# Performance work log

Hardware: AMD Instinct MI355X
Metric: run time of the kernel (lower is better)

The kernel has to match this reference:

```python
import jax, jax.numpy as jnp
import numpy as np

N = 50000      # nodes
E = 800000     # edges
D_IN = 128     # embedding_in
EP = 200000    # prediction edge pairs
CONV_DIMS = [D_IN, 128, 64, 32]
LIN_DIMS = [32, 16, 8, 1]


def setup_inputs() -> dict:
    key = jax.random.key(0)
    ks = jax.random.split(key, 20)
    inp = {
        "x": jax.random.normal(ks[0], (N, D_IN), dtype=jnp.float32),
        "edge_index": jax.random.randint(ks[1], (2, E), 0, N, dtype=jnp.int64 if jax.config.jax_enable_x64 else jnp.int32),
        "pred_edges": jax.random.randint(ks[2], (EP, 2), 0, N, dtype=jnp.int64 if jax.config.jax_enable_x64 else jnp.int32),
    }
    k = 3
    for i in range(3):  # GCNConv weights [in,out] + bias (torch GCNConv has bias)
        din, dout = CONV_DIMS[i], CONV_DIMS[i + 1]
        inp[f"cw{i}"] = jax.random.normal(ks[k], (din, dout), dtype=jnp.float32) / np.sqrt(din); k += 1
        inp[f"cb{i}"] = jax.random.normal(ks[k], (dout,), dtype=jnp.float32) * 0.01; k += 1
    for i in range(3):  # Linear weights stored [in,out]
        din, dout = LIN_DIMS[i], LIN_DIMS[i + 1]
        inp[f"lw{i}"] = jax.random.normal(ks[k], (din, dout), dtype=jnp.float32) / np.sqrt(din); k += 1
        inp[f"lb{i}"] = jax.random.normal(ks[k], (dout,), dtype=jnp.float32) * 0.01; k += 1
    return inp


def gcn_conv(x, W, b, src, dst, n):
    """PyG GCNConv: D^-1/2 (A + I) D^-1/2 X W + b, deg over dst incl. self-loop."""
    h = x @ W  # [n, dout]
    deg = jax.ops.segment_sum(jnp.ones_like(dst, dtype=h.dtype), dst, num_segments=n) + 1.0
    dis = jax.lax.rsqrt(deg)  # deg >= 1 (self loop)
    msg = h[src] * (dis[src] * dis[dst])[:, None]      # gather + per-edge normalize
    out = jax.ops.segment_sum(msg, dst, num_segments=n)  # scatter-add into targets
    out = out + h * (dis * dis)[:, None]                # self-loop contribution
    return out + b


def reference(x, edge_index, pred_edges, cw0, cb0, cw1, cb1, cw2, cb2,
              lw0, lb0, lw1, lb1, lw2, lb2):
    src, dst = edge_index[0], edge_index[1]
    n = x.shape[0]
    for W, b in ((cw0, cb0), (cw1, cb1), (cw2, cb2)):
        x = jax.nn.relu(gcn_conv(x, W, b, src, dst, n))
    x = jax.nn.relu(x @ lw0 + lb0)
    x = jax.nn.relu(x @ lw1 + lb1)
    x = jax.nn.sigmoid(x @ lw2 + lb2)  # [n, 1]
    s = x[:, 0]
    # x[pred_edges] -> [EP,2,1]; mul of pair, transpose+flatten -> [EP]
    return s[pred_edges[:, 0]] * s[pred_edges[:, 1]]
```

## Files before the change

### kernel.cpp

```cpp
#include <hip/hip_runtime.h>
#include <math.h>

constexpr int NN  = 50000;
constexpr int NP  = 50048;
constexpr int NE  = 800000;
constexpr int NEP = 200000;

constexpr int NBKT  = 256;
constexpr int CAP   = 4096;
constexpr int CAPC  = 4096;
constexpr int CHUNK = 4096;

constexpr int BKB = (NE + CHUNK - 1) / CHUNK;
constexpr int W0B = 128 * 128 / 256;
constexpr int W1B = 128 * 64 / 256;
constexpr int W2B = 64 * 32 / 256;
constexpr int FRONT_BLOCKS = BKB + W0B + W1B + W2B;

constexpr int NODE_BLKS32 = (NN + 31) / 32;
constexpr int NODE_BLKS16 = (NN + 15) / 16;

typedef _Float16 half8_t __attribute__((ext_vector_type(8)));
typedef float    float4_t __attribute__((ext_vector_type(4)));

static inline int cdiv(long long a, int b) { return (int)((a + b - 1) / b); }

__global__ __launch_bounds__(256) void k_front(const int* __restrict__ src,
        const int* __restrict__ dst, int* __restrict__ binCnt,
        unsigned int* __restrict__ ebuf,
        const float* __restrict__ cw0, _Float16* __restrict__ WT0,
        const float* __restrict__ cw1, _Float16* __restrict__ WT1,
        const float* __restrict__ cw2, _Float16* __restrict__ WT2) {
    const int tid = threadIdx.x;
    const int bid = blockIdx.x;

    if (bid < BKB) {
        __shared__ int hist[NBKT];
        __shared__ int base[NBKT];
        __shared__ int cur[NBKT];
        constexpr int J = CHUNK / 256;
        const int e0 = bid * CHUNK;
        hist[tid] = 0;
        __syncthreads();
        int  s[J], bn[J], dl[J];
        bool ok[J];
#pragma unroll
        for (int j = 0; j < J; ++j) {
            int i = e0 + j * 256 + tid;
            ok[j] = i < NE;
            if (ok[j]) {
                int d = dst[i];
                s[j]  = src[i];
                bn[j] = d >> 8;
                dl[j] = d & 255;
                atomicAdd(&hist[bn[j]], 1);
            }
        }
        __syncthreads();
        base[tid] = hist[tid] ? atomicAdd(&binCnt[tid], hist[tid]) : 0;
        cur[tid] = 0;
        __syncthreads();
#pragma unroll
        for (int j = 0; j < J; ++j) {
            if (ok[j]) {
                int slot = base[bn[j]] + atomicAdd(&cur[bn[j]], 1);
                ebuf[bn[j] * CAP + slot] = (unsigned int)s[j] | ((unsigned int)dl[j] << 16);
            }
        }
        return;
    }
    if (bid < BKB + W0B) {
        int idx = (bid - BKB) * 256 + tid;
        int k = idx >> 7, n = idx & 127;
        WT0[(size_t)n * 128 + k] = (_Float16)cw0[idx];
        return;
    }
    if (bid < BKB + W0B + W1B) {
        int idx = (bid - BKB - W0B) * 256 + tid;
        int k = idx >> 6, n = idx & 63;
        WT1[(size_t)n * 128 + k] = (_Float16)cw1[idx];
        return;
    }
    {
        int idx = (bid - BKB - W0B - W1B) * 256 + tid;
        int k = idx >> 5, n = idx & 31;
        WT2[(size_t)n * 64 + k] = (_Float16)cw2[idx];
    }
}

__global__ __launch_bounds__(256) void k_csrbuild(const unsigned int* __restrict__ ebuf,
        const int* __restrict__ binCnt, int* __restrict__ off, float* __restrict__ dis,
        unsigned short* __restrict__ csr) {
    __shared__ int hist[256];
    __shared__ int sh[256];
    __shared__ int cur[256];
    const int tid = threadIdx.x;
    const int bin = blockIdx.x;
    const int cnt = binCnt[bin];
    const unsigned int* eb = ebuf + (size_t)bin * CAP;

    hist[tid] = 0;
    __syncthreads();
    for (int i = tid; i < cnt; i += 256)
        atomicAdd(&hist[eb[i] >> 16], 1);
    __syncthreads();

    int v  = hist[tid];
    int pv = (v + 3) & ~3;
    sh[tid] = pv;
    __syncthreads();
    for (int d = 1; d < 256; d <<= 1) {
        int t = (tid >= d) ? sh[tid - d] : 0;
        __syncthreads();
        sh[tid] += t;
        __syncthreads();
    }
    int start = bin * CAPC + (sh[tid] - pv);

    int node = bin * 256 + tid;
    if (node < NN) {
        off[node] = start | (pv << 20);
        dis[node] = rsqrtf((float)v + 1.0f);
    }
    cur[tid] = start;
    __syncthreads();

    for (int i = tid; i < cnt; i += 256) {
        unsigned int e = eb[i];
        int p = atomicAdd(&cur[e >> 16], 1);
        csr[p] = (unsigned short)(e & 0xFFFFu);
    }
    for (int k2 = v; k2 < pv; ++k2) csr[start + k2] = (unsigned short)NN;
}

__global__ __launch_bounds__(256) void k_gemm0(const float* __restrict__ X,
        const _Float16* __restrict__ WT, const float* __restrict__ dis,
        _Float16* __restrict__ g, int n) {
    constexpr int K = 128, DOUT = 128;
    constexpr int NC = 64, NT = 4, KT = 4, MT = 2;

    const int tid  = threadIdx.x;
    const int L    = tid & 63;
    const int w    = tid >> 6;
    const int wc   = w & 1;
    const int wr   = w >> 1;
    const int r0   = blockIdx.x * 64 + wr * 32;
    const int c0   = wc * NC;
    const int quad = L >> 4;
    const int lm   = L & 15;

    float4_t acc[MT][NT];
#pragma unroll
    for (int mt = 0; mt < MT; ++mt)
#pragma unroll
        for (int nt = 0; nt < NT; ++nt) acc[mt][nt] = (float4_t){0.f, 0.f, 0.f, 0.f};

#pragma unroll
    for (int kt = 0; kt < KT; ++kt) {
        half8_t a[MT], b[NT];
#pragma unroll
        for (int mt = 0; mt < MT; ++mt) {
            const float* xr = X + (size_t)(r0 + mt * 16 + lm) * K + kt * 32 + quad * 8;
            float4 u = *(const float4*)xr;
            float4 v = *(const float4*)(xr + 4);
            a[mt] = (half8_t){(_Float16)u.x, (_Float16)u.y, (_Float16)u.z, (_Float16)u.w,
                              (_Float16)v.x, (_Float16)v.y, (_Float16)v.z, (_Float16)v.w};
        }
#pragma unroll
        for (int nt = 0; nt < NT; ++nt)
            b[nt] = *(const half8_t*)(WT + (size_t)(c0 + nt * 16 + lm) * K + kt * 32 + quad * 8);
#pragma unroll
        for (int mt = 0; mt < MT; ++mt)
#pragma unroll
            for (int nt = 0; nt < NT; ++nt)
                acc[mt][nt] = __builtin_amdgcn_mfma_f32_16x16x32_f16(a[mt], b[nt], acc[mt][nt], 0, 0, 0);
    }

#pragma unroll
    for (int mt = 0; mt < MT; ++mt) {
        int rb = r0 + mt * 16 + quad * 4;
        float dv[4];
        *(float4*)dv = *(const float4*)(dis + rb);
#pragma unroll
        for (int nt = 0; nt < NT; ++nt) {
            int c = c0 + nt * 16 + lm;
#pragma unroll
            for (int reg = 0; reg < 4; ++reg) {
                int r = rb + reg;
                if (r < n)       g[(size_t)r * DOUT + c] = (_Float16)(acc[mt][nt][reg] * dv[reg]);
                else if (r == n) g[(size_t)r * DOUT + c] = (_Float16)0.f;
            }
        }
    }
}

__global__ __launch_bounds__(256) void k_agg_gemm16(const half8_t* __restrict__ gin,
        const float* __restrict__ dis, const float* __restrict__ bias,
        const int* __restrict__ off, const unsigned short* __restrict__ csr,
        const _Float16* __restrict__ WT, _Float16* __restrict__ gout, int n) {
    constexpr int DIN = 128, DOUT = 64;
    constexpr int R8 = DIN / 8;
    constexpr int XS = DIN + 8;
    __shared__ _Float16 sX[16 * XS];

    const int tid  = threadIdx.x;
    const int l16  = tid & 15;
    const int ln   = tid >> 4;
    const int r0   = blockIdx.x * 16;
    const int node = r0 + ln;

    if (blockIdx.x == 0 && tid < DOUT / 8)
        ((half8_t*)(gout + (size_t)n * DOUT))[tid] =
            (half8_t){(_Float16)0.f, (_Float16)0.f, (_Float16)0.f, (_Float16)0.f,
                      (_Float16)0.f, (_Float16)0.f, (_Float16)0.f, (_Float16)0.f};

    float dd = dis[node];
    half8_t hv = gin[(size_t)node * R8 + l16];
    float a[8];
#pragma unroll
    for (int j = 0; j < 8; ++j) a[j] = (float)hv[j];

    int pk = off[node];
    int e0 = pk & 0xFFFFF;
    int e1 = e0 + (pk >> 20);
    int e = e0;
    for (; e + 7 < e1; e += 8) {
        ushort4 c4 = *(const ushort4*)(csr + e);
        ushort4 c8 = *(const ushort4*)(csr + e + 4);
        half8_t v0 = gin[(size_t)c4.x * R8 + l16];
        half8_t v1 = gin[(size_t)c4.y * R8 + l16];
        half8_t v2 = gin[(size_t)c4.z * R8 + l16];
        half8_t v3 = gin[(size_t)c4.w * R8 + l16];
        half8_t v4 = gin[(size_t)c8.x * R8 + l16];
        half8_t v5 = gin[(size_t)c8.y * R8 + l16];
        half8_t v6 = gin[(size_t)c8.z * R8 + l16];
        half8_t v7 = gin[(size_t)c8.w * R8 + l16];
#pragma unroll
        for (int j = 0; j < 8; ++j)
            a[j] += ((float)v0[j] + (float)v1[j]) + ((float)v2[j] + (float)v3[j])
                  + ((float)v4[j] + (float)v5[j]) + ((float)v6[j] + (float)v7[j]);
    }
    if (e < e1) {
        ushort4 c4 = *(const ushort4*)(csr + e);
        half8_t v0 = gin[(size_t)c4.x * R8 + l16];
        half8_t v1 = gin[(size_t)c4.y * R8 + l16];
        half8_t v2 = gin[(size_t)c4.z * R8 + l16];
        half8_t v3 = gin[(size_t)c4.w * R8 + l16];
#pragma unroll
        for (int j = 0; j < 8; ++j)
            a[j] += ((float)v0[j] + (float)v1[j]) + ((float)v2[j] + (float)v3[j]);
    }
    {
        half8_t o;
#pragma unroll
        for (int j = 0; j < 8; ++j)
            o[j] = (_Float16)fmaxf(fmaf(a[j], dd, bias[l16 * 8 + j]), 0.f);
        *(half8_t*)(sX + ln * XS + l16 * 8) = o;
    }
    __syncthreads();

    const int L    = tid & 63;
    const int w    = tid >> 6;
    const int quad = L >> 4;
    const int lm   = L & 15;
    const int c0   = w * 16;

    float4_t acc = (float4_t){0.f, 0.f, 0.f, 0.f};
#pragma unroll
    for (int kt = 0; kt < DIN / 32; ++kt) {
        half8_t b  = *(const half8_t*)(WT + (size_t)(c0 + lm) * DIN + kt * 32 + quad * 8);
        half8_t aF = *(const half8_t*)(sX + lm * XS + kt * 32 + quad * 8);
        acc = __builtin_amdgcn_mfma_f32_16x16x32_f16(aF, b, acc, 0, 0, 0);
    }
    int rb = r0 + quad * 4;
    float dv[4];
    *(float4*)dv = *(const float4*)(dis + rb);
#pragma unroll
    for (int reg = 0; reg < 4; ++reg)
        gout[(size_t)(rb + reg) * DOUT + c0 + lm] = (_Float16)(acc[reg] * dv[reg]);
}

__global__ __launch_bounds__(256) void k_agg_gemm8(const half8_t* __restrict__ gin,
        const float* __restrict__ dis, const float* __restrict__ bias,
        const int* __restrict__ off, const unsigned short* __restrict__ csr,
        const _Float16* __restrict__ WT, _Float16* __restrict__ gout, int n) {
    constexpr int DIN = 64, DOUT = 32;
    constexpr int R8 = DIN / 8;
    constexpr int XS = DIN + 8;
    __shared__ _Float16 sX[32 * XS];

    const int tid  = threadIdx.x;
    const int l8   = tid & 7;
    const int ln   = tid >> 3;
    const int r0   = blockIdx.x * 32;
    const int node = r0 + ln;

    if (node < n) {
        float dd = dis[node];
        half8_t hv = gin[(size_t)node * R8 + l8];
        float a[8];
#pragma unroll
        for (int j = 0; j < 8; ++j) a[j] = (float)hv[j];
        int pk = off[node];
        int e0 = pk & 0xFFFFF;
        int e1 = e0 + (pk >> 20);
        int e = e0;
        for (; e + 7 < e1; e += 8) {
            ushort4 c4 = *(const ushort4*)(csr + e);
            ushort4 c8 = *(const ushort4*)(csr + e + 4);
            half8_t v0 = gin[(size_t)c4.x * R8 + l8];
            half8_t v1 = gin[(size_t)c4.y * R8 + l8];
            half8_t v2 = gin[(size_t)c4.z * R8 + l8];
            half8_t v3 = gin[(size_t)c4.w * R8 + l8];
            half8_t v4 = gin[(size_t)c8.x * R8 + l8];
            half8_t v5 = gin[(size_t)c8.y * R8 + l8];
            half8_t v6 = gin[(size_t)c8.z * R8 + l8];
            half8_t v7 = gin[(size_t)c8.w * R8 + l8];
#pragma unroll
            for (int j = 0; j < 8; ++j)
                a[j] += ((float)v0[j] + (float)v1[j]) + ((float)v2[j] + (float)v3[j])
                      + ((float)v4[j] + (float)v5[j]) + ((float)v6[j] + (float)v7[j]);
        }
        if (e < e1) {
            ushort4 c4 = *(const ushort4*)(csr + e);
            half8_t v0 = gin[(size_t)c4.x * R8 + l8];
            half8_t v1 = gin[(size_t)c4.y * R8 + l8];
            half8_t v2 = gin[(size_t)c4.z * R8 + l8];
            half8_t v3 = gin[(size_t)c4.w * R8 + l8];
#pragma unroll
            for (int j = 0; j < 8; ++j)
                a[j] += ((float)v0[j] + (float)v1[j]) + ((float)v2[j] + (float)v3[j]);
        }
        half8_t o;
#pragma unroll
        for (int j = 0; j < 8; ++j)
            o[j] = (_Float16)fmaxf(fmaf(a[j], dd, bias[l8 * 8 + j]), 0.f);
        *(half8_t*)(sX + ln * XS + l8 * 8) = o;
    } else {
        *(half8_t*)(sX + ln * XS + l8 * 8) =
            (half8_t){(_Float16)0.f, (_Float16)0.f, (_Float16)0.f, (_Float16)0.f,
                      (_Float16)0.f, (_Float16)0.f, (_Float16)0.f, (_Float16)0.f};
    }
    __syncthreads();

    const int L    = tid & 63;
    const int w    = tid >> 6;
    const int quad = L >> 4;
    const int lm   = L & 15;
    const int c0   = (w & 1) * 16;
    const int m0   = (w >> 1) * 16;

    float4_t acc = (float4_t){0.f, 0.f, 0.f, 0.f};
#pragma unroll
    for (int kt = 0; kt < DIN / 32; ++kt) {
        half8_t b  = *(const half8_t*)(WT + (size_t)(c0 + lm) * DIN + kt * 32 + quad * 8);
        half8_t aF = *(const half8_t*)(sX + (m0 + lm) * XS + kt * 32 + quad * 8);
        acc = __builtin_amdgcn_mfma_f32_16x16x32_f16(aF, b, acc, 0, 0, 0);
    }
    int rb = r0 + m0 + quad * 4;
    float dv[4];
    *(float4*)dv = *(const float4*)(dis + rb);
#pragma unroll
    for (int reg = 0; reg < 4; ++reg) {
        int r = rb + reg;
        if (r < n)       gout[(size_t)r * DOUT + c0 + lm] = (_Float16)(acc[reg] * dv[reg]);
        else if (r == n) gout[(size_t)r * DOUT + c0 + lm] = (_Float16)0.f;
    }
}

__global__ __launch_bounds__(256) void k_agg_mlp(const half8_t* __restrict__ g,
        const float* __restrict__ dis, const float* __restrict__ b,
        const int* __restrict__ off, const unsigned short* __restrict__ csr,
        const float* __restrict__ lw0, const float* __restrict__ lb0,
        const float* __restrict__ lw1, const float* __restrict__ lb1,
        const float* __restrict__ lw2, const float* __restrict__ lb2,
        float* __restrict__ sv, int n) {
    __shared__ float sh[32 * 33];
    const int tid  = threadIdx.x;
    const int l8   = tid & 7;
    const int lane = l8 & 3;
    const int grp  = l8 >> 2;
    const int ln   = tid >> 3;
    const int node = blockIdx.x * 32 + ln;

    if (node < n) {
        float dd = dis[node];
        half8_t hv = g[(size_t)node * 4 + lane];
        float a[8];
#pragma unroll
        for (int j = 0; j < 8; ++j) a[j] = (grp == 0) ? (float)hv[j] : 0.f;
        int pk = off[node];
        int e0 = pk & 0xFFFFF;
        int e1 = e0 + (pk >> 20);
        for (int e = e0 + grp * 4; e < e1; e += 8) {
            ushort4 c4 = *(const ushort4*)(csr + e);
            half8_t v0 = g[(size_t)c4.x * 4 + lane];
            half8_t v1 = g[(size_t)c4.y * 4 + lane];
            half8_t v2 = g[(size_t)c4.z * 4 + lane];
            half8_t v3 = g[(size_t)c4.w * 4 + lane];
#pragma unroll
            for (int j = 0; j < 8; ++j)
                a[j] += (float)v0[j] + (float)v1[j] + (float)v2[j] + (float)v3[j];
        }
#pragma unroll
        for (int j = 0; j < 8; ++j) a[j] += __shfl_xor(a[j], 4);
        if (grp == 0) {
            float* row = sh + ln * 33 + lane * 8;
#pragma unroll
            for (int j = 0; j < 8; ++j)
                row[j] = fmaxf(fmaf(a[j], dd, b[lane * 8 + j]), 0.f);
        }
    }
    __syncthreads();

    if (tid < 32) {
        int node2 = blockIdx.x * 32 + tid;
        if (node2 < n) {
            const float* v = sh + tid * 33;
            float a[16];
#pragma unroll
            for (int j = 0; j < 16; ++j) {
                float acc = lb0[j];
#pragma unroll
                for (int k = 0; k < 32; ++k) acc = fmaf(v[k], lw0[k * 16 + j], acc);
                a[j] = fmaxf(acc, 0.f);
            }
            float b8[8];
#pragma unroll
            for (int j = 0; j < 8; ++j) {
                float acc = lb1[j];
#pragma unroll
                for (int k = 0; k < 16; ++k) acc = fmaf(a[k], lw1[k * 8 + j], acc);
                b8[j] = fmaxf(acc, 0.f);
            }
            float z = lb2[0];
#pragma unroll
            for (int k = 0; k < 8; ++k) z = fmaf(b8[k], lw2[k], z);
            sv[node2] = 1.0f / (1.0f + expf(-z));
        }
    }
}

__global__ void k_pred(const float* __restrict__ s, const int* __restrict__ pe,
                       float* __restrict__ out, int ep2) {
    int i = blockIdx.x * blockDim.x + threadIdx.x;
    if (i >= ep2) return;
    int4 p = ((const int4*)pe)[i];
    float2 o;
    o.x = s[p.x] * s[p.y];
    o.y = s[p.z] * s[p.w];
    ((float2*)out)[i] = o;
}

extern "C" void kernel_launch(void* const* d_in, const int* in_sizes, int n_in,
                              void* d_out, int out_size, void* d_ws, size_t ws_size,
                              hipStream_t stream) {
    const float* x   = (const float*)d_in[0];
    const int*   ei  = (const int*)d_in[1];
    const int*   pe  = (const int*)d_in[2];
    const float* cw0 = (const float*)d_in[3];
    const float* cb0 = (const float*)d_in[4];
    const float* cw1 = (const float*)d_in[5];
    const float* cb1 = (const float*)d_in[6];
    const float* cw2 = (const float*)d_in[7];
    const float* cb2 = (const float*)d_in[8];
    const float* lw0 = (const float*)d_in[9];
    const float* lb0 = (const float*)d_in[10];
    const float* lw1 = (const float*)d_in[11];
    const float* lb1 = (const float*)d_in[12];
    const float* lw2 = (const float*)d_in[13];
    const float* lb2 = (const float*)d_in[14];

    const int* src = ei;
    const int* dst = ei + NE;

    char* w = (char*)d_ws;
    float*          dis  = (float*)w;           w += sizeof(float) * NN;
    _Float16*       M0   = (_Float16*)w;        w += sizeof(_Float16) * (size_t)(NN + 1) * 128;
    _Float16*       M1   = (_Float16*)w;        w += sizeof(_Float16) * (size_t)(NN + 1) * 64;
    _Float16*       M2   = (_Float16*)w;        w += sizeof(_Float16) * (size_t)(NN + 1) * 32;
    float*          sv   = (float*)w;           w += sizeof(float) * NN;
    _Float16*       WT0  = (_Float16*)w;        w += sizeof(_Float16) * 128 * 128;
    _Float16*       WT1  = (_Float16*)w;        w += sizeof(_Float16) * 64 * 128;
    _Float16*       WT2  = (_Float16*)w;        w += sizeof(_Float16) * 32 * 64;
    int*            off  = (int*)w;             w += sizeof(int) * NN;
    unsigned short* csr  = (unsigned short*)w;  w += sizeof(unsigned short) * (size_t)NBKT * CAPC;
    int*            binCnt = (int*)w;           w += sizeof(int) * NBKT;
    unsigned int*   ebuf = (unsigned int*)w;    w += sizeof(unsigned int) * (size_t)NBKT * CAP;

    const int T = 256;

    hipMemsetAsync(binCnt, 0, sizeof(int) * NBKT, stream);
    k_front<<<FRONT_BLOCKS, 256, 0, stream>>>(src, dst, binCnt, ebuf,
                                              cw0, WT0, cw1, WT1, cw2, WT2);

    k_csrbuild<<<NBKT, 256, 0, stream>>>(ebuf, binCnt, off, dis, csr);

    k_gemm0<<<NP / 64, 256, 0, stream>>>(x, WT0, dis, M0, NN);

    k_agg_gemm16<<<NODE_BLKS16, 256, 0, stream>>>((const half8_t*)M0, dis, cb0,
                                                  off, csr, WT1, M1, NN);

    k_agg_gemm8<<<NODE_BLKS32, 256, 0, stream>>>((const half8_t*)M1, dis, cb1,
                                                 off, csr, WT2, M2, NN);

    k_agg_mlp<<<NODE_BLKS32, 256, 0, stream>>>((const half8_t*)M2, dis, cb2, off, csr,
                                               lw0, lb0, lw1, lb1, lw2, lb2, sv, NN);

    k_pred<<<cdiv(NEP / 2, T), T, 0, stream>>>(sv, pe, (float*)d_out, NEP / 2);
}
```

Measured before the change: 213.2 us.

## Renumber nodes by in-degree so aggregation warps get balanced neighbor counts

Adds a degree histogram in the CSR build plus two new kernels that rank nodes by in-degree (counting sort) and remap CSR neighbor ids into the permuted numbering. gemm0 writes rows in permuted order, the aggregation kernels index the permuted offsets and scaling arrays, and the final MLP scatters back to original node ids. The aim is to group nodes of similar degree in the same wavefront, cutting divergence and load imbalance in the gather loops. The cost is two extra launches, a full pass over the CSR, and scattered writes in gemm0 and the MLP output.

```diff
diff --git a/kernel.cpp b/kernel.cpp
--- a/kernel.cpp
+++ b/kernel.cpp
@@ -19,6 +19,7 @@
 
 constexpr int NODE_BLKS32 = (NN + 31) / 32;
 constexpr int NODE_BLKS16 = (NN + 15) / 16;
+constexpr int NDEG = 128;
 
 typedef _Float16 half8_t __attribute__((ext_vector_type(8)));
 typedef float    float4_t __attribute__((ext_vector_type(4)));
@@ -90,16 +91,19 @@
 
 __global__ __launch_bounds__(256) void k_csrbuild(const unsigned int* __restrict__ ebuf,
         const int* __restrict__ binCnt, int* __restrict__ off, float* __restrict__ dis,
-        unsigned short* __restrict__ csr) {
+        unsigned short* __restrict__ csr, unsigned char* __restrict__ deg8,
+        int* __restrict__ degHist) {
     __shared__ int hist[256];
     __shared__ int sh[256];
     __shared__ int cur[256];
+    __shared__ int dh[NDEG];
     const int tid = threadIdx.x;
     const int bin = blockIdx.x;
     const int cnt = binCnt[bin];
     const unsigned int* eb = ebuf + (size_t)bin * CAP;
 
     hist[tid] = 0;
+    if (tid < NDEG) dh[tid] = 0;
     __syncthreads();
     for (int i = tid; i < cnt; i += 256)
         atomicAdd(&hist[eb[i] >> 16], 1);
@@ -121,6 +125,9 @@
     if (node < NN) {
         off[node] = start | (pv << 20);
         dis[node] = rsqrtf((float)v + 1.0f);
+        int dc = v < NDEG - 1 ? v : NDEG - 1;
+        deg8[node] = (unsigned char)dc;
+        atomicAdd(&dh[dc], 1);
     }
     cur[tid] = start;
     __syncthreads();
@@ -131,11 +138,66 @@
         csr[p] = (unsigned short)(e & 0xFFFFu);
     }
     for (int k2 = v; k2 < pv; ++k2) csr[start + k2] = (unsigned short)NN;
+    __syncthreads();
+    if (tid < NDEG && dh[tid]) atomicAdd(&degHist[tid], dh[tid]);
+}
+
+__global__ __launch_bounds__(256) void k_rank(const unsigned char* __restrict__ deg8,
+        const int* __restrict__ off, const float* __restrict__ dis,
+        const int* __restrict__ degHist, int* __restrict__ degCur,
+        unsigned short* __restrict__ perm16, int* __restrict__ off_p,
+        float* __restrict__ disp, unsigned short* __restrict__ orig16) {
+    __shared__ int gbase[NDEG];
+    __shared__ int lhist[NDEG];
+    __shared__ int lbase[NDEG];
+    const int tid  = threadIdx.x;
+    const int node = blockIdx.x * 256 + tid;
+
+    if (tid < NDEG) gbase[tid] = degHist[tid];
+    __syncthreads();
+    for (int d = 1; d < NDEG; d <<= 1) {
+        int t = (tid < NDEG && tid >= d) ? gbase[tid - d] : 0;
+        __syncthreads();
+        if (tid < NDEG) gbase[tid] += t;
+        __syncthreads();
+    }
+    if (tid < NDEG) gbase[tid] -= degHist[tid];
+    if (tid < NDEG) lhist[tid] = 0;
+    __syncthreads();
+
+    int d = -1, li = 0;
+    if (node < NN) {
+        d  = deg8[node];
+        li = atomicAdd(&lhist[d], 1);
+    }
+    __syncthreads();
+    if (tid < NDEG) lbase[tid] = lhist[tid] ? atomicAdd(&degCur[tid], lhist[tid]) : 0;
+    __syncthreads();
+
+    if (node < NN) {
+        int rank = gbase[d] + lbase[d] + li;
+        perm16[node] = (unsigned short)rank;
+        off_p[rank]  = off[node];
+        disp[rank]   = dis[node];
+        orig16[rank] = (unsigned short)node;
+    }
+    if (node == NN) perm16[NN] = (unsigned short)NN;
+}
+
+__global__ __launch_bounds__(256) void k_remap(unsigned short* __restrict__ csr,
+        const unsigned short* __restrict__ perm16) {
+    const int idx = blockIdx.x * 256 + threadIdx.x;
+    uint4 v = ((uint4*)csr)[idx];
+    unsigned int r0 = perm16[v.x & 0xFFFFu] | ((unsigned int)perm16[v.x >> 16] << 16);
+    unsigned int r1 = perm16[v.y & 0xFFFFu] | ((unsigned int)perm16[v.y >> 16] << 16);
+    unsigned int r2 = perm16[v.z & 0xFFFFu] | ((unsigned int)perm16[v.z >> 16] << 16);
+    unsigned int r3 = perm16[v.w & 0xFFFFu] | ((unsigned int)perm16[v.w >> 16] << 16);
+    ((uint4*)csr)[idx] = make_uint4(r0, r1, r2, r3);
 }
 
 __global__ __launch_bounds__(256) void k_gemm0(const float* __restrict__ X,
         const _Float16* __restrict__ WT, const float* __restrict__ dis,
-        _Float16* __restrict__ g, int n) {
+        const unsigned short* __restrict__ perm16, _Float16* __restrict__ g, int n) {
     constexpr int K = 128, DOUT = 128;
     constexpr int NC = 64, NT = 4, KT = 4, MT = 2;
 
@@ -187,16 +249,20 @@
 #pragma unroll
             for (int reg = 0; reg < 4; ++reg) {
                 int r = rb + reg;
-                if (r < n)       g[(size_t)r * DOUT + c] = (_Float16)(acc[mt][nt][reg] * dv[reg]);
-                else if (r == n) g[(size_t)r * DOUT + c] = (_Float16)0.f;
+                if (r < n) {
+                    int pr = perm16[r];
+                    g[(size_t)pr * DOUT + c] = (_Float16)(acc[mt][nt][reg] * dv[reg]);
+                } else if (r == n) {
+                    g[(size_t)n * DOUT + c] = (_Float16)0.f;
+                }
             }
         }
     }
 }
 
 __global__ __launch_bounds__(256) void k_agg_gemm16(const half8_t* __restrict__ gin,
-        const float* __restrict__ dis, const float* __restrict__ bias,
-        const int* __restrict__ off, const unsigned short* __restrict__ csr,
+        const float* __restrict__ disp, const float* __restrict__ bias,
+        const int* __restrict__ off_p, const unsigned short* __restrict__ csr,
         const _Float16* __restrict__ WT, _Float16* __restrict__ gout, int n) {
     constexpr int DIN = 128, DOUT = 64;
     constexpr int R8 = DIN / 8;
@@ -214,13 +280,13 @@
             (half8_t){(_Float16)0.f, (_Float16)0.f, (_Float16)0.f, (_Float16)0.f,
                       (_Float16)0.f, (_Float16)0.f, (_Float16)0.f, (_Float16)0.f};
 
-    float dd = dis[node];
+    float dd = disp[node];
     half8_t hv = gin[(size_t)node * R8 + l16];
     float a[8];
 #pragma unroll
     for (int j = 0; j < 8; ++j) a[j] = (float)hv[j];
 
-    int pk = off[node];
+    int pk = off_p[node];
     int e0 = pk & 0xFFFFF;
     int e1 = e0 + (pk >> 20);
     int e = e0;
@@ -274,15 +340,15 @@
     }
     int rb = r0 + quad * 4;
     float dv[4];
-    *(float4*)dv = *(const float4*)(dis + rb);
+    *(float4*)dv = *(const float4*)(disp + rb);
 #pragma unroll
     for (int reg = 0; reg < 4; ++reg)
         gout[(size_t)(rb + reg) * DOUT + c0 + lm] = (_Float16)(acc[reg] * dv[reg]);
 }
 
 __global__ __launch_bounds__(256) void k_agg_gemm8(const half8_t* __restrict__ gin,
-        const float* __restrict__ dis, const float* __restrict__ bias,
-        const int* __restrict__ off, const unsigned short* __restrict__ csr,
+        const float* __restrict__ disp, const float* __restrict__ bias,
+        const int* __restrict__ off_p, const unsigned short* __restrict__ csr,
         const _Float16* __restrict__ WT, _Float16* __restrict__ gout, int n) {
     constexpr int DIN = 64, DOUT = 32;
     constexpr int R8 = DIN / 8;
@@ -296,12 +362,12 @@
     const int node = r0 + ln;
 
     if (node < n) {
-        float dd = dis[node];
+        float dd = disp[node];
         half8_t hv = gin[(size_t)node * R8 + l8];
         float a[8];
 #pragma unroll
         for (int j = 0; j < 8; ++j) a[j] = (float)hv[j];
-        int pk = off[node];
+        int pk = off_p[node];
         int e0 = pk & 0xFFFFF;
         int e1 = e0 + (pk >> 20);
         int e = e0;
@@ -359,7 +425,7 @@
     }
     int rb = r0 + m0 + quad * 4;
     float dv[4];
-    *(float4*)dv = *(const float4*)(dis + rb);
+    *(float4*)dv = *(const float4*)(disp + rb);
 #pragma unroll
     for (int reg = 0; reg < 4; ++reg) {
         int r = rb + reg;
@@ -369,8 +435,9 @@
 }
 
 __global__ __launch_bounds__(256) void k_agg_mlp(const half8_t* __restrict__ g,
-        const float* __restrict__ dis, const float* __restrict__ b,
-        const int* __restrict__ off, const unsigned short* __restrict__ csr,
+        const float* __restrict__ disp, const float* __restrict__ b,
+        const int* __restrict__ off_p, const unsigned short* __restrict__ csr,
+        const unsigned short* __restrict__ orig16,
         const float* __restrict__ lw0, const float* __restrict__ lb0,
         const float* __restrict__ lw1, const float* __restrict__ lb1,
         const float* __restrict__ lw2, const float* __restrict__ lb2,
@@ -384,12 +451,12 @@
     const int node = blockIdx.x * 32 + ln;
 
     if (node < n) {
-        float dd = dis[node];
+        float dd = disp[node];
         half8_t hv = g[(size_t)node * 4 + lane];
         float a[8];
 #pragma unroll
         for (int j = 0; j < 8; ++j) a[j] = (grp == 0) ? (float)hv[j] : 0.f;
-        int pk = off[node];
+        int pk = off_p[node];
         int e0 = pk & 0xFFFFF;
         int e1 = e0 + (pk >> 20);
         for (int e = e0 + grp * 4; e < e1; e += 8) {
@@ -436,7 +503,7 @@
             float z = lb2[0];
 #pragma unroll
             for (int k = 0; k < 8; ++k) z = fmaf(b8[k], lw2[k], z);
-            sv[node2] = 1.0f / (1.0f + expf(-z));
+            sv[orig16[node2]] = 1.0f / (1.0f + expf(-z));
         }
     }
 }
@@ -475,37 +542,51 @@
     const int* dst = ei + NE;
 
     char* w = (char*)d_ws;
-    float*          dis  = (float*)w;           w += sizeof(float) * NN;
-    _Float16*       M0   = (_Float16*)w;        w += sizeof(_Float16) * (size_t)(NN + 1) * 128;
-    _Float16*       M1   = (_Float16*)w;        w += sizeof(_Float16) * (size_t)(NN + 1) * 64;
-    _Float16*       M2   = (_Float16*)w;        w += sizeof(_Float16) * (size_t)(NN + 1) * 32;
-    float*          sv   = (float*)w;           w += sizeof(float) * NN;
-    _Float16*       WT0  = (_Float16*)w;        w += sizeof(_Float16) * 128 * 128;
-    _Float16*       WT1  = (_Float16*)w;        w += sizeof(_Float16) * 64 * 128;
-    _Float16*       WT2  = (_Float16*)w;        w += sizeof(_Float16) * 32 * 64;
-    int*            off  = (int*)w;             w += sizeof(int) * NN;
-    unsigned short* csr  = (unsigned short*)w;  w += sizeof(unsigned short) * (size_t)NBKT * CAPC;
-    int*            binCnt = (int*)w;           w += sizeof(int) * NBKT;
-    unsigned int*   ebuf = (unsigned int*)w;    w += sizeof(unsigned int) * (size_t)NBKT * CAP;
+    float*          dis   = (float*)w;           w += sizeof(float) * NN;
+    _Float16*       M0    = (_Float16*)w;        w += sizeof(_Float16) * (size_t)(NN + 1) * 128;
+    _Float16*       M1    = (_Float16*)w;        w += sizeof(_Float16) * (size_t)(NN + 1) * 64;
+    _Float16*       M2    = (_Float16*)w;        w += sizeof(_Float16) * (size_t)(NN + 1) * 32;
+    float*          sv    = (float*)w;           w += sizeof(float) * NN;
+    _Float16*       WT0   = (_Float16*)w;        w += sizeof(_Float16) * 128 * 128;
+    _Float16*       WT1   = (_Float16*)w;        w += sizeof(_Float16) * 64 * 128;
+    _Float16*       WT2   = (_Float16*)w;        w += sizeof(_Float16) * 32 * 64;
+    int*            off   = (int*)w;             w += sizeof(int) * NN;
+    int*            off_p = (int*)w;             w += sizeof(int) * NN;
+    float*          disp  = (float*)w;           w += sizeof(float) * NN;
+    unsigned short* csr   = (unsigned short*)w;  w += sizeof(unsigned short) * (size_t)NBKT * CAPC;
+    unsigned short* perm16 = (unsigned short*)w; w += sizeof(unsigned short) * 65536;
+    unsigned short* orig16 = (unsigned short*)w; w += sizeof(unsigned short) * NN;
+    unsigned char*  deg8  = (unsigned char*)w;   w += NN;
+    w = (char*)(((size_t)w + 15) & ~(size_t)15);
+    int*            zeroZ = (int*)w;             w += sizeof(int) * (NBKT + 2 * NDEG);
+    unsigned int*   ebuf  = (unsigned int*)w;    w += sizeof(unsigned int) * (size_t)NBKT * CAP;
+
+    int* binCnt  = zeroZ;
+    int* degHist = zeroZ + NBKT;
+    int* degCur  = zeroZ + NBKT + NDEG;
 
     const int T = 256;
 
-    hipMemsetAsync(binCnt, 0, sizeof(int) * NBKT, stream);
+    hipMemsetAsync(zeroZ, 0, sizeof(int) * (NBKT + 2 * NDEG), stream);
     k_front<<<FRONT_BLOCKS, 256, 0, stream>>>(src, dst, binCnt, ebuf,
                                               cw0, WT0, cw1, WT1, cw2, WT2);
 
-    k_csrbuild<<<NBKT, 256, 0, stream>>>(ebuf, binCnt, off, dis, csr);
-
-    k_gemm0<<<NP / 64, 256, 0, stream>>>(x, WT0, dis, M0, NN);
-
-    k_agg_gemm16<<<NODE_BLKS16, 256, 0, stream>>>((const half8_t*)M0, dis, cb0,
-                                                  off, csr, WT1, M1, NN);
-
-    k_agg_gemm8<<<NODE_BLKS32, 256, 0, stream>>>((const half8_t*)M1, dis, cb1,
-                                                 off, csr, WT2, M2, NN);
-
-    k_agg_mlp<<<NODE_BLKS32, 256, 0, stream>>>((const half8_t*)M2, dis, cb2, off, csr,
-                                               lw0, lb0, lw1, lb1, lw2, lb2, sv, NN);
+    k_csrbuild<<<NBKT, 256, 0, stream>>>(ebuf, binCnt, off, dis, csr, deg8, degHist);
+
+    k_rank<<<cdiv(NN + 1, 256), 256, 0, stream>>>(deg8, off, dis, degHist, degCur,
+                                                  perm16, off_p, disp, orig16);
+    k_remap<<<(NBKT * CAPC / 8) / 256, 256, 0, stream>>>(csr, perm16);
+
+    k_gemm0<<<NP / 64, 256, 0, stream>>>(x, WT0, dis, perm16, M0, NN);
+
+    k_agg_gemm16<<<NODE_BLKS16, 256, 0, stream>>>((const half8_t*)M0, disp, cb0,
+                                                  off_p, csr, WT1, M1, NN);
+
+    k_agg_gemm8<<<NODE_BLKS32, 256, 0, stream>>>((const half8_t*)M1, disp, cb1,
+                                                 off_p, csr, WT2, M2, NN);
+
+    k_agg_mlp<<<NODE_BLKS32, 256, 0, stream>>>((const half8_t*)M2, disp, cb2, off_p, csr,
+                                               orig16, lw0, lb0, lw1, lb1, lw2, lb2, sv, NN);
 
     k_pred<<<cdiv(NEP / 2, T), T, 0, stream>>>(sv, pe, (float*)d_out, NEP / 2);
 }
```

Result: slower. 228.7 us (+7.3%).

## Split each node's edge gather across two lane groups in layer-1 aggregation

Applied to the files above, without the earlier changes.

The first aggregate+GEMM kernel now runs 512 threads per block. Two 16-lane groups share each node, each taking alternating 4-edge chunks of its neighbour list, and the partial sums are combined with a cross-lane xor shuffle. The aim is more memory-level parallelism in the irregular gather and less per-thread serial latency on high-degree nodes. In exchange, half the threads sit idle during the MFMA stage, the larger blocks may lower occupancy, and the residency pattern of the CSR reads changes.

```diff
diff --git a/kernel.cpp b/kernel.cpp
--- a/kernel.cpp
+++ b/kernel.cpp
@@ -194,7 +194,7 @@
     }
 }
 
-__global__ __launch_bounds__(256) void k_agg_gemm16(const half8_t* __restrict__ gin,
+__global__ __launch_bounds__(512) void k_agg_gemm16(const half8_t* __restrict__ gin,
         const float* __restrict__ dis, const float* __restrict__ bias,
         const int* __restrict__ off, const unsigned short* __restrict__ csr,
         const _Float16* __restrict__ WT, _Float16* __restrict__ gout, int n) {
@@ -204,8 +204,10 @@
     __shared__ _Float16 sX[16 * XS];
 
     const int tid  = threadIdx.x;
-    const int l16  = tid & 15;
-    const int ln   = tid >> 4;
+    const int l32  = tid & 31;
+    const int l16  = l32 & 15;
+    const int grp  = l32 >> 4;
+    const int ln   = tid >> 5;
     const int r0   = blockIdx.x * 16;
     const int node = r0 + ln;
 
@@ -215,32 +217,20 @@
                       (_Float16)0.f, (_Float16)0.f, (_Float16)0.f, (_Float16)0.f};
 
     float dd = dis[node];
-    half8_t hv = gin[(size_t)node * R8 + l16];
     float a[8];
-#pragma unroll
-    for (int j = 0; j < 8; ++j) a[j] = (float)hv[j];
+    if (grp == 0) {
+        half8_t hv = gin[(size_t)node * R8 + l16];
+#pragma unroll
+        for (int j = 0; j < 8; ++j) a[j] = (float)hv[j];
+    } else {
+#pragma unroll
+        for (int j = 0; j < 8; ++j) a[j] = 0.f;
+    }
 
     int pk = off[node];
     int e0 = pk & 0xFFFFF;
     int e1 = e0 + (pk >> 20);
-    int e = e0;
-    for (; e + 7 < e1; e += 8) {
-        ushort4 c4 = *(const ushort4*)(csr + e);
-        ushort4 c8 = *(const ushort4*)(csr + e + 4);
-        half8_t v0 = gin[(size_t)c4.x * R8 + l16];
-        half8_t v1 = gin[(size_t)c4.y * R8 + l16];
-        half8_t v2 = gin[(size_t)c4.z * R8 + l16];
-        half8_t v3 = gin[(size_t)c4.w * R8 + l16];
-        half8_t v4 = gin[(size_t)c8.x * R8 + l16];
-        half8_t v5 = gin[(size_t)c8.y * R8 + l16];
-        half8_t v6 = gin[(size_t)c8.z * R8 + l16];
-        half8_t v7 = gin[(size_t)c8.w * R8 + l16];
-#pragma unroll
-        for (int j = 0; j < 8; ++j)
-            a[j] += ((float)v0[j] + (float)v1[j]) + ((float)v2[j] + (float)v3[j])
-                  + ((float)v4[j] + (float)v5[j]) + ((float)v6[j] + (float)v7[j]);
-    }
-    if (e < e1) {
+    for (int e = e0 + grp * 4; e < e1; e += 8) {
         ushort4 c4 = *(const ushort4*)(csr + e);
         half8_t v0 = gin[(size_t)c4.x * R8 + l16];
         half8_t v1 = gin[(size_t)c4.y * R8 + l16];
@@ -250,7 +240,10 @@
         for (int j = 0; j < 8; ++j)
             a[j] += ((float)v0[j] + (float)v1[j]) + ((float)v2[j] + (float)v3[j]);
     }
-    {
+#pragma unroll
+    for (int j = 0; j < 8; ++j) a[j] += __shfl_xor(a[j], 16);
+
+    if (grp == 0) {
         half8_t o;
 #pragma unroll
         for (int j = 0; j < 8; ++j)
@@ -259,25 +252,27 @@
     }
     __syncthreads();
 
-    const int L    = tid & 63;
-    const int w    = tid >> 6;
-    const int quad = L >> 4;
-    const int lm   = L & 15;
-    const int c0   = w * 16;
-
-    float4_t acc = (float4_t){0.f, 0.f, 0.f, 0.f};
-#pragma unroll
-    for (int kt = 0; kt < DIN / 32; ++kt) {
-        half8_t b  = *(const half8_t*)(WT + (size_t)(c0 + lm) * DIN + kt * 32 + quad * 8);
-        half8_t aF = *(const half8_t*)(sX + lm * XS + kt * 32 + quad * 8);
-        acc = __builtin_amdgcn_mfma_f32_16x16x32_f16(aF, b, acc, 0, 0, 0);
-    }
-    int rb = r0 + quad * 4;
-    float dv[4];
-    *(float4*)dv = *(const float4*)(dis + rb);
-#pragma unroll
-    for (int reg = 0; reg < 4; ++reg)
-        gout[(size_t)(rb + reg) * DOUT + c0 + lm] = (_Float16)(acc[reg] * dv[reg]);
+    const int w = tid >> 6;
+    if (w < 4) {
+        const int L    = tid & 63;
+        const int quad = L >> 4;
+        const int lm   = L & 15;
+        const int c0   = w * 16;
+
+        float4_t acc = (float4_t){0.f, 0.f, 0.f, 0.f};
+#pragma unroll
+        for (int kt = 0; kt < DIN / 32; ++kt) {
+            half8_t b  = *(const half8_t*)(WT + (size_t)(c0 + lm) * DIN + kt * 32 + quad * 8);
+            half8_t aF = *(const half8_t*)(sX + lm * XS + kt * 32 + quad * 8);
+            acc = __builtin_amdgcn_mfma_f32_16x16x32_f16(aF, b, acc, 0, 0, 0);
+        }
+        int rb = r0 + quad * 4;
+        float dv[4];
+        *(float4*)dv = *(const float4*)(dis + rb);
+#pragma unroll
+        for (int reg = 0; reg < 4; ++reg)
+            gout[(size_t)(rb + reg) * DOUT + c0 + lm] = (_Float16)(acc[reg] * dv[reg]);
+    }
 }
 
 __global__ __launch_bounds__(256) void k_agg_gemm8(const half8_t* __restrict__ gin,
@@ -498,7 +493,7 @@
 
     k_gemm0<<<NP / 64, 256, 0, stream>>>(x, WT0, dis, M0, NN);
 
-    k_agg_gemm16<<<NODE_BLKS16, 256, 0, stream>>>((const half8_t*)M0, dis, cb0,
+    k_agg_gemm16<<<NODE_BLKS16, 512, 0, stream>>>((const half8_t*)M0, dis, cb0,
                                                   off, csr, WT1, M1, NN);
 
     k_agg_gemm8<<<NODE_BLKS32, 256, 0, stream>>>((const half8_t*)M1, dis, cb1,
```

Measured after the change: 214.2 us. Within noise of the previous version (+0.4%).

## Sort nodes by in-degree within each bucket to balance aggregation wavefronts

Applied to the files above, without the earlier changes.

The CSR build now counting-sorts the 256 nodes of each bucket by in-degree, capped at 127, and writes a per-bucket node permutation. The three aggregation kernels take their node from this permutation, so the nodes sharing a wavefront have similar degrees and spend less time waiting on the highest-degree lane in the edge-gather loop. Each output row is then written to its permuted node index through shared-memory tables. The cost is an extra scan in the CSR build, one more indirection, and output stores that are less contiguous than before.

```diff
diff --git a/kernel.cpp b/kernel.cpp
--- a/kernel.cpp
+++ b/kernel.cpp
@@ -19,6 +19,7 @@
 
 constexpr int NODE_BLKS32 = (NN + 31) / 32;
 constexpr int NODE_BLKS16 = (NN + 15) / 16;
+constexpr int NDEG = 128;
 
 typedef _Float16 half8_t __attribute__((ext_vector_type(8)));
 typedef float    float4_t __attribute__((ext_vector_type(4)));
@@ -90,16 +91,19 @@
 
 __global__ __launch_bounds__(256) void k_csrbuild(const unsigned int* __restrict__ ebuf,
         const int* __restrict__ binCnt, int* __restrict__ off, float* __restrict__ dis,
-        unsigned short* __restrict__ csr) {
+        unsigned short* __restrict__ csr, unsigned short* __restrict__ nodeOrder) {
     __shared__ int hist[256];
     __shared__ int sh[256];
     __shared__ int cur[256];
+    __shared__ int lh[NDEG];
+    __shared__ int lhs[NDEG];
     const int tid = threadIdx.x;
     const int bin = blockIdx.x;
     const int cnt = binCnt[bin];
     const unsigned int* eb = ebuf + (size_t)bin * CAP;
 
     hist[tid] = 0;
+    if (tid < NDEG) lh[tid] = 0;
     __syncthreads();
     for (int i = tid; i < cnt; i += 256)
         atomicAdd(&hist[eb[i] >> 16], 1);
@@ -117,13 +121,29 @@
     }
     int start = bin * CAPC + (sh[tid] - pv);
 
-    int node = bin * 256 + tid;
+    const int node = bin * 256 + tid;
+    int dc = -1, li = 0;
     if (node < NN) {
         off[node] = start | (pv << 20);
         dis[node] = rsqrtf((float)v + 1.0f);
+        dc = v < NDEG - 1 ? v : NDEG - 1;
+        li = atomicAdd(&lh[dc], 1);
     }
     cur[tid] = start;
     __syncthreads();
+
+    if (tid < NDEG) lhs[tid] = lh[tid];
+    __syncthreads();
+    for (int d = 1; d < NDEG; d <<= 1) {
+        int t = (tid < NDEG && tid >= d) ? lhs[tid - d] : 0;
+        __syncthreads();
+        if (tid < NDEG) lhs[tid] += t;
+        __syncthreads();
+    }
+    if (node < NN) {
+        int rank = (lhs[dc] - lh[dc]) + li;
+        nodeOrder[bin * 256 + rank] = (unsigned short)node;
+    }
 
     for (int i = tid; i < cnt; i += 256) {
         unsigned int e = eb[i];
@@ -197,17 +217,19 @@
 __global__ __launch_bounds__(256) void k_agg_gemm16(const half8_t* __restrict__ gin,
         const float* __restrict__ dis, const float* __restrict__ bias,
         const int* __restrict__ off, const unsigned short* __restrict__ csr,
+        const unsigned short* __restrict__ nodeOrder,
         const _Float16* __restrict__ WT, _Float16* __restrict__ gout, int n) {
     constexpr int DIN = 128, DOUT = 64;
     constexpr int R8 = DIN / 8;
     constexpr int XS = DIN + 8;
     __shared__ _Float16 sX[16 * XS];
+    __shared__ int   sNode[16];
+    __shared__ float sDis[16];
 
     const int tid  = threadIdx.x;
     const int l16  = tid & 15;
     const int ln   = tid >> 4;
-    const int r0   = blockIdx.x * 16;
-    const int node = r0 + ln;
+    const int node = nodeOrder[blockIdx.x * 16 + ln];
 
     if (blockIdx.x == 0 && tid < DOUT / 8)
         ((half8_t*)(gout + (size_t)n * DOUT))[tid] =
@@ -215,6 +237,7 @@
                       (_Float16)0.f, (_Float16)0.f, (_Float16)0.f, (_Float16)0.f};
 
     float dd = dis[node];
+    if (l16 == 0) { sNode[ln] = node; sDis[ln] = dd; }
     half8_t hv = gin[(size_t)node * R8 + l16];
     float a[8];
 #pragma unroll
@@ -272,31 +295,41 @@
         half8_t aF = *(const half8_t*)(sX + lm * XS + kt * 32 + quad * 8);
         acc = __builtin_amdgcn_mfma_f32_16x16x32_f16(aF, b, acc, 0, 0, 0);
     }
-    int rb = r0 + quad * 4;
-    float dv[4];
-    *(float4*)dv = *(const float4*)(dis + rb);
-#pragma unroll
-    for (int reg = 0; reg < 4; ++reg)
-        gout[(size_t)(rb + reg) * DOUT + c0 + lm] = (_Float16)(acc[reg] * dv[reg]);
+#pragma unroll
+    for (int reg = 0; reg < 4; ++reg) {
+        int lr  = quad * 4 + reg;
+        int tgt = sNode[lr];
+        gout[(size_t)tgt * DOUT + c0 + lm] = (_Float16)(acc[reg] * sDis[lr]);
+    }
 }
 
 __global__ __launch_bounds__(256) void k_agg_gemm8(const half8_t* __restrict__ gin,
         const float* __restrict__ dis, const float* __restrict__ bias,
         const int* __restrict__ off, const unsigned short* __restrict__ csr,
+        const unsigned short* __restrict__ nodeOrder,
         const _Float16* __restrict__ WT, _Float16* __restrict__ gout, int n) {
     constexpr int DIN = 64, DOUT = 32;
     constexpr int R8 = DIN / 8;
     constexpr int XS = DIN + 8;
     __shared__ _Float16 sX[32 * XS];
+    __shared__ int   sNode[32];
+    __shared__ float sDis[32];
 
     const int tid  = threadIdx.x;
     const int l8   = tid & 7;
     const int ln   = tid >> 3;
-    const int r0   = blockIdx.x * 32;
-    const int node = r0 + ln;
-
-    if (node < n) {
+    const int slot = blockIdx.x * 32 + ln;
+    const bool act = slot < n;
+    const int node = act ? nodeOrder[slot] : 0;
+
+    if (blockIdx.x == 0 && tid < DOUT / 8)
+        ((half8_t*)(gout + (size_t)n * DOUT))[tid] =
+            (half8_t){(_Float16)0.f, (_Float16)0.f, (_Float16)0.f, (_Float16)0.f,
+                      (_Float16)0.f, (_Float16)0.f, (_Float16)0.f, (_Float16)0.f};
+
+    if (act) {
         float dd = dis[node];
+        if (l8 == 0) { sNode[ln] = node; sDis[ln] = dd; }
         half8_t hv = gin[(size_t)node * R8 + l8];
         float a[8];
 #pragma unroll
@@ -334,9 +367,10 @@
         half8_t o;
 #pragma unroll
         for (int j = 0; j < 8; ++j)
-            o[j] = (_Float16)fmaxf(fmaf(a[j], dd, bias[l8 * 8 + j]), 0.f);
+            o[j] = (_Float16)fmaxf(fmaf(a[j], sDis[ln], bias[l8 * 8 + j]), 0.f);
         *(half8_t*)(sX + ln * XS + l8 * 8) = o;
     } else {
+        if (l8 == 0) { sNode[ln] = 0x7FFFFFFF; sDis[ln] = 0.f; }
         *(half8_t*)(sX + ln * XS + l8 * 8) =
             (half8_t){(_Float16)0.f, (_Float16)0.f, (_Float16)0.f, (_Float16)0.f,
                       (_Float16)0.f, (_Float16)0.f, (_Float16)0.f, (_Float16)0.f};
@@ -357,33 +391,36 @@
         half8_t aF = *(const half8_t*)(sX + (m0 + lm) * XS + kt * 32 + quad * 8);
         acc = __builtin_amdgcn_mfma_f32_16x16x32_f16(aF, b, acc, 0, 0, 0);
     }
-    int rb = r0 + m0 + quad * 4;
-    float dv[4];
-    *(float4*)dv = *(const float4*)(dis + rb);
 #pragma unroll
     for (int reg = 0; reg < 4; ++reg) {
-        int r = rb + reg;
-        if (r < n)       gout[(size_t)r * DOUT + c0 + lm] = (_Float16)(acc[reg] * dv[reg]);
-        else if (r == n) gout[(size_t)r * DOUT + c0 + lm] = (_Float16)0.f;
+        int lr  = m0 + quad * 4 + reg;
+        int tgt = sNode[lr];
+        if (tgt < n)
+            gout[(size_t)tgt * DOUT + c0 + lm] = (_Float16)(acc[reg] * sDis[lr]);
     }
 }
 
 __global__ __launch_bounds__(256) void k_agg_mlp(const half8_t* __restrict__ g,
         const float* __restrict__ dis, const float* __restrict__ b,
         const int* __restrict__ off, const unsigned short* __restrict__ csr,
+        const unsigned short* __restrict__ nodeOrder,
         const float* __restrict__ lw0, const float* __restrict__ lb0,
         const float* __restrict__ lw1, const float* __restrict__ lb1,
         const float* __restrict__ lw2, const float* __restrict__ lb2,
         float* __restrict__ sv, int n) {
     __shared__ float sh[32 * 33];
+    __shared__ int sNode[32];
     const int tid  = threadIdx.x;
     const int l8   = tid & 7;
     const int lane = l8 & 3;
     const int grp  = l8 >> 2;
     const int ln   = tid >> 3;
-    const int node = blockIdx.x * 32 + ln;
-
-    if (node < n) {
+    const int slot = blockIdx.x * 32 + ln;
+    const bool act = slot < n;
+    const int node = act ? nodeOrder[slot] : 0;
+
+    if (act) {
+        if (l8 == 0) sNode[ln] = node;
         float dd = dis[node];
         half8_t hv = g[(size_t)node * 4 + lane];
         float a[8];
@@ -410,12 +447,14 @@
             for (int j = 0; j < 8; ++j)
                 row[j] = fmaxf(fmaf(a[j], dd, b[lane * 8 + j]), 0.f);
         }
+    } else if (l8 == 0) {
+        sNode[ln] = 0x7FFFFFFF;
     }
     __syncthreads();
 
     if (tid < 32) {
-        int node2 = blockIdx.x * 32 + tid;
-        if (node2 < n) {
+        int tgt = sNode[tid];
+        if (tgt < n) {
             const float* v = sh + tid * 33;
             float a[16];
 #pragma unroll
@@ -436,7 +475,7 @@
             float z = lb2[0];
 #pragma unroll
             for (int k = 0; k < 8; ++k) z = fmaf(b8[k], lw2[k], z);
-            sv[node2] = 1.0f / (1.0f + expf(-z));
+            sv[tgt] = 1.0f / (1.0f + expf(-z));
         }
     }
 }
@@ -485,6 +524,7 @@
     _Float16*       WT2  = (_Float16*)w;        w += sizeof(_Float16) * 32 * 64;
     int*            off  = (int*)w;             w += sizeof(int) * NN;
     unsigned short* csr  = (unsigned short*)w;  w += sizeof(unsigned short) * (size_t)NBKT * CAPC;
+    unsigned short* nodeOrder = (unsigned short*)w; w += sizeof(unsigned short) * (size_t)NBKT * 256;
     int*            binCnt = (int*)w;           w += sizeof(int) * NBKT;
     unsigned int*   ebuf = (unsigned int*)w;    w += sizeof(unsigned int) * (size_t)NBKT * CAP;
 
@@ -494,18 +534,18 @@
     k_front<<<FRONT_BLOCKS, 256, 0, stream>>>(src, dst, binCnt, ebuf,
                                               cw0, WT0, cw1, WT1, cw2, WT2);
 
-    k_csrbuild<<<NBKT, 256, 0, stream>>>(ebuf, binCnt, off, dis, csr);
+    k_csrbuild<<<NBKT, 256, 0, stream>>>(ebuf, binCnt, off, dis, csr, nodeOrder);
 
     k_gemm0<<<NP / 64, 256, 0, stream>>>(x, WT0, dis, M0, NN);
 
     k_agg_gemm16<<<NODE_BLKS16, 256, 0, stream>>>((const half8_t*)M0, dis, cb0,
-                                                  off, csr, WT1, M1, NN);
+                                                  off, csr, nodeOrder, WT1, M1, NN);
 
     k_agg_gemm8<<<NODE_BLKS32, 256, 0, stream>>>((const half8_t*)M1, dis, cb1,
-                                                 off, csr, WT2, M2, NN);
+                                                 off, csr, nodeOrder, WT2, M2, NN);
 
     k_agg_mlp<<<NODE_BLKS32, 256, 0, stream>>>((const half8_t*)M2, dis, cb2, off, csr,
-                                               lw0, lb0, lw1, lb1, lw2, lb2, sv, NN);
+                                               nodeOrder, lw0, lb0, lw1, lb1, lw2, lb2, sv, NN);
 
     k_pred<<<cdiv(NEP / 2, T), T, 0, stream>>>(sv, pe, (float*)d_out, NEP / 2);
 }
```

Measured after the change: 231.8 us. 1.09x slower.
